# Optimization experiments

Measured on AMD Instinct MI355X. Metric: run time of the kernel, lower is better.

## Reference

```python
import jax, jax.numpy as jnp
import numpy as np

L, H, NH, B, S = 6, 768, 12, 4, 1024
D = H // NH
SCALE = 1.0 / np.sqrt(D)
EPS = 1e-5


def setup_inputs() -> dict:
    key = jax.random.key(0)
    ks = jax.random.split(key, 20)
    std = np.sqrt(2.0 / (5.0 * H)).astype(np.float32)
    w = lambda k, shape: (jax.random.normal(k, shape, jnp.float32) * std)
    x = jax.random.normal(ks[0], (B, S, H), jnp.float32)
    lengths = jnp.array([1024, 896, 768, 640])  # no fully-masked rows
    pad_mask = jnp.arange(S)[None, :] >= lengths[:, None]  # True = padding
    inp = {
        "x": x,
        "pad_mask": pad_mask,
        "Wq": w(ks[1], (L, H, H)), "bq": jnp.zeros((L, H), jnp.float32),
        "Wk": w(ks[2], (L, H, H)), "bk": w(ks[3], (L, H)) * 0.1,
        "Wv": w(ks[4], (L, H, H)), "bv": w(ks[5], (L, H)) * 0.1,
        "Wo": w(ks[6], (L, H, H)), "bo": jnp.zeros((L, H), jnp.float32),
        "ln1_g": jnp.ones((L, H), jnp.float32), "ln1_b": jnp.zeros((L, H), jnp.float32),
        "ln2_g": jnp.ones((L, H), jnp.float32), "ln2_b": jnp.zeros((L, H), jnp.float32),
        "W1": w(ks[7], (L, 8 * H, H)), "b1": jnp.zeros((L, 8 * H), jnp.float32),
        "W2": w(ks[8], (L, H, 4 * H)), "b2": jnp.zeros((L, H), jnp.float32),
        "out_g": jnp.ones((H,), jnp.float32), "out_b": jnp.zeros((H,), jnp.float32),
    }
    return inp


def _ln(x, g, b):
    m = jnp.mean(x, axis=-1, keepdims=True)
    v = jnp.mean(jnp.square(x - m), axis=-1, keepdims=True)
    return (x - m) * jax.lax.rsqrt(v + EPS) * g + b


def _encoder(x, pad_mask, params):
    def layer(x, p):
        (Wq, bq, Wk, bk, Wv, bv, Wo, bo, g1, be1, g2, be2, W1, b1, W2, b2) = p
        Bz, Sl, Hd = x.shape
        xn = _ln(x, g1, be1)
        q = (xn @ Wq.T + bq).reshape(Bz, Sl, NH, D)
        k = (xn @ Wk.T + bk).reshape(Bz, Sl, NH, D)
        v = (xn @ Wv.T + bv).reshape(Bz, Sl, NH, D)
        scores = jnp.einsum('bqhd,bkhd->bhqk', q, k) * SCALE
        scores = jnp.where(pad_mask[:, None, None, :], -jnp.inf, scores)
        probs = jax.nn.softmax(scores, axis=-1)
        av = jnp.einsum('bhqk,bkhd->bqhd', probs, v).reshape(Bz, Sl, Hd)
        x = x + (av @ Wo.T + bo)
        xn = _ln(x, g2, be2)
        h = xn @ W1.T + b1
        u, gate = jnp.split(h, 2, axis=-1)
        x = x + (u * jax.nn.gelu(gate, approximate=False)) @ W2.T + b2
        return x, None

    x, _ = jax.lax.scan(layer, x, params)
    return x


def reference(x, pad_mask, Wq, bq, Wk, bk, Wv, bv, Wo, bo,
              ln1_g, ln1_b, ln2_g, ln2_b, W1, b1, W2, b2, out_g, out_b):
    params = (Wq, bq, Wk, bk, Wv, bv, Wo, bo,
              ln1_g, ln1_b, ln2_g, ln2_b, W1, b1, W2, b2)
    x = _encoder(x, pad_mask, params)
    return _ln(x, out_g, out_b)
```

## Files before the change

### kernel.cpp

```cpp
#include <hip/hip_runtime.h>

typedef unsigned short u16;
typedef __bf16 bf16x8 __attribute__((ext_vector_type(8)));
typedef unsigned short us8 __attribute__((ext_vector_type(8)));
typedef unsigned short us4 __attribute__((ext_vector_type(4)));
typedef float f32x4 __attribute__((ext_vector_type(4)));

typedef __attribute__((address_space(3))) unsigned int as3_uint;
typedef const __attribute__((address_space(1))) unsigned int as1_cuint;

__device__ __forceinline__ u16 f2bf(float f) {
    unsigned u = __float_as_uint(f);
    u += 0x7FFFu + ((u >> 16) & 1u);
    return (u16)(u >> 16);
}
__device__ __forceinline__ float bf2f(u16 h) {
    return __uint_as_float(((unsigned)h) << 16);
}
__device__ __forceinline__ bf16x8 ld8(const u16* p) {
    return __builtin_bit_cast(bf16x8, *(const us8*)p);
}
#define MFMA16(a, b, c) __builtin_amdgcn_mfma_f32_16x16x32_bf16(a, b, c, 0, 0, 0)

__device__ __forceinline__ void glds16(const void* g, void* l) {
    __builtin_amdgcn_global_load_lds((as1_cuint*)g, (as3_uint*)l, 16, 0, 0);
}

__global__ void detect_k(const unsigned* __restrict__ pm, int* __restrict__ len4) {
    __shared__ int isbool;
    const int t = threadIdx.x;
    if (t == 0) isbool = 0;
    __syncthreads();
    unsigned orv = pm[t] | pm[256 + t] | pm[512 + t] | pm[768 + t];
    if (orv & 0xFFFFFF00u) atomicOr(&isbool, 1);
    __syncthreads();
    const int w = t >> 6, l = t & 63;
    int cnt = 0;
    if (isbool) {
        const unsigned char* p8 = (const unsigned char*)pm;
        for (int i = l; i < 1024; i += 64) cnt += (p8[w * 1024 + i] == 0) ? 1 : 0;
    } else {
        for (int i = l; i < 1024; i += 64) cnt += (pm[w * 1024 + i] == 0u) ? 1 : 0;
    }
#pragma unroll
    for (int m = 1; m < 64; m <<= 1) cnt += __shfl_xor(cnt, m);
    if (l == 0) {
        int c = cnt;
        if (c < 1) c = 1;
        if (c > 1024) c = 1024;
        len4[w] = c;
    }
}

__global__ __launch_bounds__(256) void conv_k(
    const float* __restrict__ Wq, const float* __restrict__ Wk,
    const float* __restrict__ Wv, const float* __restrict__ Wo,
    const float* __restrict__ W1, const float* __restrict__ W2,
    const float* __restrict__ bq, const float* __restrict__ bk,
    const float* __restrict__ bv,
    u16* __restrict__ wqkvo, u16* __restrict__ w1b, u16* __restrict__ w2b,
    float* __restrict__ bqkv, int lyr) {
    const int idx = blockIdx.x * 256 + threadIdx.x;
    const size_t e = (size_t)idx * 4;
    const float* src;
    u16* dst;
    if (e < 2359296u) {
        int which = (int)(e / 589824u);
        size_t off = e % 589824u;
        const float* m = (which == 0) ? Wq : (which == 1) ? Wk : (which == 2) ? Wv : Wo;
        src = m + (size_t)lyr * 589824u + off;
        dst = wqkvo + e;
    } else if (e < 7077888u) {
        size_t off = e - 2359296u;
        src = W1 + (size_t)lyr * 4718592u + off;
        dst = w1b + off;
    } else {
        size_t off = e - 7077888u;
        src = W2 + (size_t)lyr * 2359296u + off;
        dst = w2b + off;
    }
    float4 v = *(const float4*)src;
    us4 o;
    o[0] = f2bf(v.x); o[1] = f2bf(v.y); o[2] = f2bf(v.z); o[3] = f2bf(v.w);
    *(us4*)dst = o;
    if (idx < 2304) {
        float bb = (idx < 768) ? bq[lyr * 768 + idx]
                 : (idx < 1536) ? bk[lyr * 768 + idx - 768]
                                : bv[lyr * 768 + idx - 1536];
        bqkv[idx] = bb;
    }
}

template <int OUTF>
__global__ __launch_bounds__(256) void ln_k(const float* __restrict__ x,
                                            const float* __restrict__ gm,
                                            const float* __restrict__ bt,
                                            void* __restrict__ outp) {
    const int w = threadIdx.x >> 6, l = threadIdx.x & 63;
    const int row = blockIdx.x * 4 + w;
    const float4* xr = (const float4*)(x + (size_t)row * 768);
    float4 v[3];
    float s = 0.f, ss = 0.f;
#pragma unroll
    for (int i = 0; i < 3; ++i) {
        v[i] = xr[i * 64 + l];
        s += v[i].x + v[i].y + v[i].z + v[i].w;
        ss += v[i].x * v[i].x + v[i].y * v[i].y + v[i].z * v[i].z + v[i].w * v[i].w;
    }
#pragma unroll
    for (int m = 1; m < 64; m <<= 1) {
        s += __shfl_xor(s, m);
        ss += __shfl_xor(ss, m);
    }
    const float mean = s * (1.f / 768.f);
    float var = ss * (1.f / 768.f) - mean * mean;
    var = fmaxf(var, 0.f);
    const float rs = rsqrtf(var + 1e-5f);
    const float4* g4 = (const float4*)gm;
    const float4* b4 = (const float4*)bt;
#pragma unroll
    for (int i = 0; i < 3; ++i) {
        float4 gg = g4[i * 64 + l], bb = b4[i * 64 + l];
        float o0 = (v[i].x - mean) * rs * gg.x + bb.x;
        float o1 = (v[i].y - mean) * rs * gg.y + bb.y;
        float o2 = (v[i].z - mean) * rs * gg.z + bb.z;
        float o3 = (v[i].w - mean) * rs * gg.w + bb.w;
        if (OUTF) {
            ((float4*)outp)[(size_t)row * 192 + i * 64 + l] = make_float4(o0, o1, o2, o3);
        } else {
            us4 pk;
            pk[0] = f2bf(o0); pk[1] = f2bf(o1); pk[2] = f2bf(o2); pk[3] = f2bf(o3);
            ((us4*)outp)[(size_t)row * 192 + i * 64 + l] = pk;
        }
    }
}

template <int VAR, int NF, int CHAIN, int PRO>
__device__ __forceinline__ void g256_body(
    const u16* __restrict__ Ab, const u16* __restrict__ Bb0,
    const u16* __restrict__ Bb1,
    const u16* __restrict__ AbN, const u16* __restrict__ Bb0N,
    const u16* __restrict__ Bb1N,
    const float* __restrict__ bias, u16* __restrict__ outp,
    u16* __restrict__ vT, int ldout, int ncol0, int m0,
    u16 (&lds)[2][4][8192]) {
    const int tid = threadIdx.x;
    const int w = tid >> 6, l = tid & 63, ax = l & 15, gx = l >> 4;
    const int wr = w >> 2, wc = w & 3;
    const int K = 768;

    const int row0 = tid >> 2, cc0 = (tid & 3) ^ ((row0 >> 1) & 3);
    const int row1 = 128 + row0, cc1 = (tid & 3) ^ ((row1 >> 1) & 3);
    const size_t goA0 = (size_t)row0 * K + cc0 * 8;
    const size_t goA1 = (size_t)row1 * K + cc1 * 8;

    auto stage = [&](int u, int kt, int nxt) {
        const int kh = u & 1;
        const size_t koff = (size_t)kt * 64 + kh * 32;
        u16* d = (u16*)&lds[kt & 1][u][0];
        const u16* A_ = nxt ? AbN : Ab;
        const u16* B0_ = nxt ? Bb0N : Bb0;
        const u16* B1_ = nxt ? Bb1N : Bb1;
        if (u < 2) {
            glds16(A_ + goA0 + koff, d + tid * 8);
            glds16(A_ + goA1 + koff, d + (512 + tid) * 8);
        } else {
            glds16(B0_ + goA0 + koff, d + tid * 8);
            glds16(B1_ + goA1 + koff, d + (512 + tid) * 8);
        }
    };

    bf16x8 rav[4], rbv[NF];
    f32x4 acc[8][NF] = {};

    auto phase = [&](int buf, int q, int kh, int readB, int vm, int su, int skt,
                     int nxt) {
        if (vm == 8) asm volatile("s_waitcnt vmcnt(8)" ::: "memory");
        else if (vm == 4) asm volatile("s_waitcnt vmcnt(4)" ::: "memory");
        else if (vm == 0) asm volatile("s_waitcnt vmcnt(0)" ::: "memory");
        __builtin_amdgcn_s_barrier();
        if (readB) {
#pragma unroll
            for (int j = 0; j < NF; ++j) {
                int row;
                if (VAR == 0) row = wc * (16 * NF) + j * 16 + ax;
                else row = ((j >= NF / 2) ? 128 : 0) + wc * (8 * NF) +
                           (j % (NF / 2)) * 16 + ax;
                rbv[j] = ld8(&lds[buf][2 + kh][row * 32 + ((gx ^ ((row >> 1) & 3)) * 8)]);
            }
        }
#pragma unroll
        for (int mf = 0; mf < 4; ++mf) {
            int row = wr * 128 + q * 64 + mf * 16 + ax;
            rav[mf] = ld8(&lds[buf][kh][row * 32 + ((gx ^ ((row >> 1) & 3)) * 8)]);
        }
        if (su >= 0) stage(su, skt, nxt);
        asm volatile("s_waitcnt lgkmcnt(0)" ::: "memory");
        __builtin_amdgcn_sched_barrier(0);
        __builtin_amdgcn_s_setprio(1);
#pragma unroll
        for (int mf = 0; mf < 4; ++mf)
#pragma unroll
            for (int j = 0; j < NF; ++j)
                acc[q * 4 + mf][j] = MFMA16(rav[mf], rbv[j], acc[q * 4 + mf][j]);
        __builtin_amdgcn_s_setprio(0);
    };

    if (PRO) {
        stage(0, 0, 0); stage(2, 0, 0); stage(1, 0, 0);
        stage(3, 0, 0); stage(0, 1, 0); stage(2, 1, 0);
    }

#pragma unroll 1
    for (int t = 0; t < 5; ++t) {
        const int O = 2 * t + 1, E2 = 2 * t + 2, O2 = 2 * t + 3;
        phase(0, 0, 0, 1, 8, 1, O, 0);
        phase(0, 1, 0, 0, -1, 3, O, 0);
        phase(0, 0, 1, 1, 8, 0, E2, 0);
        phase(0, 1, 1, 0, -1, 2, E2, 0);
        phase(1, 0, 0, 1, 8, 1, E2, 0);
        phase(1, 1, 0, 0, -1, 3, E2, 0);
        phase(1, 0, 1, 1, 8, 0, O2, 0);
        phase(1, 1, 1, 0, -1, 2, O2, 0);
    }
    if (CHAIN) {
        phase(0, 0, 0, 1, 8, 1, 11, 0);
        phase(0, 1, 0, 0, -1, 3, 11, 0);
        phase(0, 0, 1, 1, 8, 0, 0, 1);
        phase(0, 1, 1, 0, -1, 2, 0, 1);
        phase(1, 0, 0, 1, 8, 1, 0, 1);
        phase(1, 1, 0, 0, -1, 3, 0, 1);
        phase(1, 0, 1, 1, 8, 0, 1, 1);
        phase(1, 1, 1, 0, -1, 2, 1, 1);
    } else {
        phase(0, 0, 0, 1, 8, 1, 11, 0);
        phase(0, 1, 0, 0, -1, 3, 11, 0);
        phase(0, 0, 1, 1, 8, -1, 0, 0);
        phase(0, 1, 1, 0, -1, -1, 0, 0);
        phase(1, 0, 0, 1, 4, -1, 0, 0);
        phase(1, 1, 0, 0, -1, -1, 0, 0);
        phase(1, 0, 1, 1, 0, -1, 0, 0);
        phase(1, 1, 1, 0, -1, -1, 0, 0);
    }

    const int rowb = m0 + wr * 128;
    if (VAR == 0) {
        if (ncol0 >= 1536) {
#pragma unroll
            for (int j = 0; j < NF; ++j) {
                const int col = ncol0 + wc * (16 * NF) + j * 16 + ax;
                const float bn = bias[col];
                u16* vcol = vT + (size_t)(col - 1536) * 4096;
#pragma unroll
                for (int am = 0; am < 8; ++am) {
                    const int rb_ = rowb + am * 16 + 4 * gx;
                    us4 pk;
#pragma unroll
                    for (int r = 0; r < 4; ++r) pk[r] = f2bf(acc[am][j][r] + bn);
                    *(us4*)(vcol + rb_) = pk;
                }
            }
        } else {
#pragma unroll
            for (int j = 0; j < NF; ++j) {
                const int col = ncol0 + wc * (16 * NF) + j * 16 + ax;
                const float bn = bias[col];
#pragma unroll
                for (int am = 0; am < 8; ++am) {
                    const int rb_ = rowb + am * 16 + 4 * gx;
#pragma unroll
                    for (int r = 0; r < 4; ++r)
                        outp[(size_t)(rb_ + r) * ldout + col] = f2bf(acc[am][j][r] + bn);
                }
            }
        }
    } else {
        const int P = NF / 2;
#pragma unroll
        for (int nf = 0; nf < NF / 2; ++nf) {
            const int col = ncol0 + wc * (16 * P) + nf * 16 + ax;
            const float bu_ = bias[col], bg_ = bias[3072 + col];
#pragma unroll
            for (int am = 0; am < 8; ++am) {
                const int rb_ = rowb + am * 16 + 4 * gx;
#pragma unroll
                for (int r = 0; r < 4; ++r) {
                    float uu = acc[am][nf][r] + bu_;
                    float gg = acc[am][P + nf][r] + bg_;
                    float gel = 0.5f * gg * (1.f + erff(gg * 0.70710678118f));
                    outp[(size_t)(rb_ + r) * ldout + col] = f2bf(uu * gel);
                }
            }
        }
    }
}

__global__ __launch_bounds__(512, 2) void qkv256_k(
    const u16* __restrict__ A, const u16* __restrict__ W,
    const float* __restrict__ bias, u16* __restrict__ outp,
    u16* __restrict__ vT) {
    __shared__ __align__(16) u16 lds[2][4][8192];
    const int bid = blockIdx.x;
    const int swz = (bid & 7) * 24 + (bid >> 3);
    const int nb = swz >> 4, mb = swz & 15;
    const int m0 = mb * 256;
    const u16* Ab = A + (size_t)m0 * 768;
    const u16* Bb0 = W + (size_t)(nb * 192) * 768;
    g256_body<0, 3, 0, 1>(Ab, Bb0, Bb0, nullptr, nullptr, nullptr,
                          bias, outp, vT, 2304, nb * 192, m0, lds);
}

__global__ __launch_bounds__(512, 2) void ffn1_k(
    const u16* __restrict__ A, const u16* __restrict__ W,
    const float* __restrict__ bias, u16* __restrict__ outp) {
    __shared__ __align__(16) u16 lds[2][4][8192];
    const int bid = blockIdx.x;
    const int swz = (bid & 7) * 32 + (bid >> 3);
    const int nb = swz >> 4, mb = swz & 15;
    const int m0 = mb * 256;
    const u16* Ab = A + (size_t)m0 * 768;
    const u16* Bb0 = W + (size_t)(nb * 128) * 768;
    const u16* Bb1 = W + (size_t)(3072 + nb * 128 - 128) * 768;
    const u16* Bb0h = W + (size_t)(2048 + nb * 64) * 768;
    const u16* Bb1h = W + (size_t)(5120 + nb * 64 - 128) * 768;
    g256_body<1, 4, 1, 1>(Ab, Bb0, Bb1, Ab, Bb0h, Bb1h,
                          bias, outp, nullptr, 3072, nb * 128, m0, lds);
    g256_body<1, 2, 0, 0>(Ab, Bb0h, Bb1h, nullptr, nullptr, nullptr,
                          bias, outp, nullptr, 3072, 2048 + nb * 64, m0, lds);
}

template <int EPI>
__global__ __launch_bounds__(512) void gemm_k(
    const u16* __restrict__ A, const u16* __restrict__ W,
    const float* __restrict__ bias, const float* __restrict__ resid,
    void* __restrict__ outp, int N, int K) {
    __shared__ __align__(16) u16 As[2][128 * 64];
    __shared__ __align__(16) u16 Bs[2][128 * 64];
    const int tid = threadIdx.x;
    const int w = tid >> 6, l = tid & 63, a = l & 15, g = l >> 4;
    const int wr = w >> 2, wc = w & 3;
    const int m0 = blockIdx.y * 128, n0 = blockIdx.x * 128;
    f32x4 acc[4][2] = {};
    const int nk = K >> 6;

    auto stage = [&](int kt, int buf) {
        const int k0 = kt * 64;
#pragma unroll
        for (int i = 0; i < 2; ++i) {
            int c = i * 512 + tid;
            int row = c >> 3, cc = c & 7, c8 = cc ^ (row & 7);
            glds16(A + (size_t)(m0 + row) * K + k0 + c8 * 8, &As[buf][c * 8]);
        }
#pragma unroll
        for (int i = 0; i < 2; ++i) {
            int c = i * 512 + tid;
            int row = c >> 3, cc = c & 7, c8 = cc ^ (row & 7);
            glds16(W + (size_t)(n0 + row) * K + k0 + c8 * 8, &Bs[buf][c * 8]);
        }
    };

    stage(0, 0);
    int cur = 0;
    for (int kt = 0; kt < nk; ++kt) {
        if (kt + 1 < nk) {
            stage(kt + 1, cur ^ 1);
            __builtin_amdgcn_sched_barrier(0);
            asm volatile("s_waitcnt vmcnt(4)" ::: "memory");
        } else {
            __builtin_amdgcn_sched_barrier(0);
            asm volatile("s_waitcnt vmcnt(0)" ::: "memory");
        }
        __builtin_amdgcn_s_barrier();
#pragma unroll
        for (int ks = 0; ks < 2; ++ks) {
            bf16x8 af[4], bv_[2];
#pragma unroll
            for (int m = 0; m < 4; ++m) {
                int row = wr * 64 + m * 16 + a;
                af[m] = ld8(&As[cur][row * 64 + (((ks * 4 + g) ^ (a & 7)) * 8)]);
            }
#pragma unroll
            for (int n = 0; n < 2; ++n) {
                int row = wc * 32 + n * 16 + a;
                bv_[n] = ld8(&Bs[cur][row * 64 + (((ks * 4 + g) ^ (a & 7)) * 8)]);
            }
#pragma unroll
            for (int m = 0; m < 4; ++m)
#pragma unroll
                for (int n = 0; n < 2; ++n)
                    acc[m][n] = MFMA16(af[m], bv_[n], acc[m][n]);
        }
        __builtin_amdgcn_s_barrier();
        cur ^= 1;
    }
    u16* outu = (u16*)outp;
    float* outf = (float*)outp;
    const int row0 = m0 + wr * 64, col0 = n0 + wc * 32;
#pragma unroll
    for (int n = 0; n < 2; ++n) {
        const int col = col0 + n * 16 + a;
        const float bn = bias[col];
#pragma unroll
        for (int m = 0; m < 4; ++m) {
            const int rb = row0 + m * 16 + 4 * g;
#pragma unroll
            for (int r = 0; r < 4; ++r) {
                const size_t off = (size_t)(rb + r) * N + col;
                float vv = acc[m][n][r] + bn;
                if constexpr (EPI == 0) {
                    outu[off] = f2bf(vv);
                } else {
                    outf[off] = vv + resid[off];
                }
            }
        }
    }
}

__global__ __launch_bounds__(256) void attn_k(const u16* __restrict__ qkv,
                                              const u16* __restrict__ vT,
                                              u16* __restrict__ av,
                                              const int* __restrict__ len4) {
    __shared__ __align__(16) u16 Ks[64 * 64];
    __shared__ __align__(16) u16 Vt[64 * 64];
    __shared__ __align__(16) u16 Ps[4][16 * 64];
    const int tid = threadIdx.x;
    const int w = tid >> 6, l = tid & 63, a = l & 15, g = l >> 4;
    const int qb = blockIdx.x, h = blockIdx.y, b = blockIdx.z;
    const size_t rowQ = (size_t)(b * 1024 + qb * 64 + w * 16 + a);
    const u16* qp = qkv + rowQ * 2304 + h * 64;
    bf16x8 qf[2];
    qf[0] = __builtin_bit_cast(bf16x8, *(const us8*)(qp + g * 8));
    qf[1] = __builtin_bit_cast(bf16x8, *(const us8*)(qp + 32 + g * 8));
    f32x4 O[4] = {};
    float m_r[4], l_r[4];
#pragma unroll
    for (int r = 0; r < 4; ++r) { m_r[r] = -1e30f; l_r[r] = 0.f; }
    const int length = len4[b];
    const int nkt = (length + 63) >> 6;
    for (int kt = 0; kt < nkt; ++kt) {
        __syncthreads();
#pragma unroll
        for (int i = 0; i < 2; ++i) {
            int c = i * 256 + tid;
            int row = c >> 3, cc = c & 7, c8 = cc ^ (row & 7);
            glds16(qkv + (size_t)(b * 1024 + kt * 64 + row) * 2304 + 768 + h * 64 + c8 * 8,
                   &Ks[c * 8]);
        }
        {
            const int d = l;
            const u16* vrow = vT + (size_t)(h * 64 + d) * 4096 + b * 1024 + kt * 64;
#pragma unroll
            for (int i = 0; i < 2; ++i) {
                int kkc = w + 4 * i;
                us8 vv = *(const us8*)(vrow + kkc * 8);
                int cc = kkc ^ (d & 7);
                *(us8*)&Vt[d * 64 + cc * 8] = vv;
            }
        }
        __syncthreads();
        f32x4 s[4] = {};
#pragma unroll
        for (int ks = 0; ks < 2; ++ks) {
#pragma unroll
            for (int f = 0; f < 4; ++f) {
                int row = f * 16 + a;
                bf16x8 kf = ld8(&Ks[row * 64 + (((ks * 4 + g) ^ (a & 7)) * 8)]);
                s[f] = MFMA16(qf[ks], kf, s[f]);
            }
        }
        float mloc[4] = {-1e30f, -1e30f, -1e30f, -1e30f};
#pragma unroll
        for (int f = 0; f < 4; ++f) {
            int kkg = kt * 64 + f * 16 + a;
            bool valid = kkg < length;
#pragma unroll
            for (int r = 0; r < 4; ++r) {
                float v = valid ? s[f][r] * 0.125f : -1e30f;
                s[f][r] = v;
                mloc[r] = fmaxf(mloc[r], v);
            }
        }
#pragma unroll
        for (int r = 0; r < 4; ++r) {
#pragma unroll
            for (int m = 1; m < 16; m <<= 1)
                mloc[r] = fmaxf(mloc[r], __shfl_xor(mloc[r], m));
        }
        float al[4], ps[4];
#pragma unroll
        for (int r = 0; r < 4; ++r) {
            float nm = fmaxf(m_r[r], mloc[r]);
            al[r] = __expf(m_r[r] - nm);
            m_r[r] = nm;
            ps[r] = 0.f;
        }
#pragma unroll
        for (int f = 0; f < 4; ++f)
#pragma unroll
            for (int r = 0; r < 4; ++r) {
                float p = __expf(s[f][r] - m_r[r]);
                s[f][r] = p;
                ps[r] += p;
            }
#pragma unroll
        for (int r = 0; r < 4; ++r) {
#pragma unroll
            for (int m = 1; m < 16; m <<= 1) ps[r] += __shfl_xor(ps[r], m);
            l_r[r] = l_r[r] * al[r] + ps[r];
        }
#pragma unroll
        for (int df = 0; df < 4; ++df)
#pragma unroll
            for (int r = 0; r < 4; ++r) O[df][r] *= al[r];
#pragma unroll
        for (int f = 0; f < 4; ++f)
#pragma unroll
            for (int r = 0; r < 4; ++r) {
                int prow = 4 * g + r;
                int cc = (2 * f + (a >> 3)) ^ (prow & 7);
                Ps[w][prow * 64 + cc * 8 + (a & 7)] = f2bf(s[f][r]);
            }
        asm volatile("s_waitcnt lgkmcnt(0)" ::: "memory");
        __builtin_amdgcn_sched_barrier(0);
#pragma unroll
        for (int ks = 0; ks < 2; ++ks) {
            bf16x8 pf = ld8(&Ps[w][a * 64 + (((ks * 4 + g) ^ (a & 7)) * 8)]);
#pragma unroll
            for (int df = 0; df < 4; ++df) {
                int vrow = df * 16 + a;
                bf16x8 vf = ld8(&Vt[vrow * 64 + (((ks * 4 + g) ^ (a & 7)) * 8)]);
                O[df] = MFMA16(pf, vf, O[df]);
            }
        }
    }
#pragma unroll
    for (int df = 0; df < 4; ++df) {
        int col = h * 64 + df * 16 + a;
#pragma unroll
        for (int r = 0; r < 4; ++r) {
            int row = b * 1024 + qb * 64 + w * 16 + 4 * g + r;
            av[(size_t)row * 768 + col] = f2bf(O[df][r] / l_r[r]);
        }
    }
}

extern "C" void kernel_launch(void* const* d_in, const int* in_sizes, int n_in,
                              void* d_out, int out_size, void* d_ws, size_t ws_size,
                              hipStream_t stream) {
    const float* x_in = (const float*)d_in[0];
    const unsigned* pm = (const unsigned*)d_in[1];
    const float* Wq = (const float*)d_in[2];
    const float* bq = (const float*)d_in[3];
    const float* Wk = (const float*)d_in[4];
    const float* bk = (const float*)d_in[5];
    const float* Wv = (const float*)d_in[6];
    const float* bv = (const float*)d_in[7];
    const float* Wo = (const float*)d_in[8];
    const float* bo = (const float*)d_in[9];
    const float* g1 = (const float*)d_in[10];
    const float* be1 = (const float*)d_in[11];
    const float* g2 = (const float*)d_in[12];
    const float* be2 = (const float*)d_in[13];
    const float* W1 = (const float*)d_in[14];
    const float* b1 = (const float*)d_in[15];
    const float* W2 = (const float*)d_in[16];
    const float* b2 = (const float*)d_in[17];
    const float* og = (const float*)d_in[18];
    const float* ob = (const float*)d_in[19];

    char* ws = (char*)d_ws;
    u16* wqkvo = (u16*)(ws + 0);
    u16* w1b   = (u16*)(ws + 4718592);
    u16* w2b   = (u16*)(ws + 14155776);
    float* bqkv = (float*)(ws + 18874368);
    int* len4  = (int*)(ws + 18883584);
    float* xbuf = (float*)(ws + 18883840);
    u16* xn    = (u16*)(ws + 31466752);
    u16* qkv   = (u16*)(ws + 37758208);
    u16* avb   = (u16*)(ws + 56632576);
    u16* ub    = (u16*)(ws + 62924032);
    u16* vT    = (u16*)(ws + 62924032);

    detect_k<<<1, 256, 0, stream>>>(pm, len4);
    for (int l = 0; l < 6; ++l) {
        conv_k<<<9216, 256, 0, stream>>>(Wq, Wk, Wv, Wo, W1, W2, bq, bk, bv,
                                         wqkvo, w1b, w2b, bqkv, l);
        const float* xcur = (l == 0) ? x_in : xbuf;
        ln_k<0><<<1024, 256, 0, stream>>>(xcur, g1 + l * 768, be1 + l * 768, xn);
        qkv256_k<<<192, 512, 0, stream>>>(xn, wqkvo, bqkv, qkv, vT);
        attn_k<<<dim3(16, 12, 4), 256, 0, stream>>>(qkv, vT, avb, len4);
        gemm_k<1><<<dim3(6, 32), 512, 0, stream>>>(avb, wqkvo + 3 * 589824, bo + l * 768,
                                                   xcur, xbuf, 768, 768);
        ln_k<0><<<1024, 256, 0, stream>>>(xbuf, g2 + l * 768, be2 + l * 768, xn);
        ffn1_k<<<256, 512, 0, stream>>>(xn, w1b, b1 + l * 6144, ub);
        gemm_k<1><<<dim3(6, 32), 512, 0, stream>>>(ub, w2b, b2 + l * 768, xbuf,
                                                   xbuf, 768, 3072);
    }
    ln_k<1><<<1024, 256, 0, stream>>>(xbuf, og, ob, d_out);
}
```

Measured before the change: 1.256 ms.

## Batch weight conversion, retile FFN1 as 1024-thread kernel, split-K gemm epilogue

All six layers' weights are now converted to bf16 in one launch before the layer loop, replacing six per-layer conversion launches, at the cost of a much larger workspace. FFN1 is rewritten as a single 1024-thread block that computes 256x192 up and gate tiles together, with a double-buffered LDS pipeline and a fused GELU epilogue. The output-projection and FFN2 gemm now split each 64-wide k-step across wave pairs, each wave holding a 64x64 tile, and the two partial sums are reduced through LDS before the epilogue. The aim is to cut launch overhead and raise MFMA density per LDS load, but it adds LDS round-trips and register pressure.

```diff
diff --git a/kernel.cpp b/kernel.cpp
--- a/kernel.cpp
+++ b/kernel.cpp
@@ -58,27 +58,22 @@
     const float* __restrict__ W1, const float* __restrict__ W2,
     const float* __restrict__ bq, const float* __restrict__ bk,
     const float* __restrict__ bv,
-    u16* __restrict__ wqkvo, u16* __restrict__ w1b, u16* __restrict__ w2b,
-    float* __restrict__ bqkv, int lyr) {
+    u16* __restrict__ wall, float* __restrict__ bqkv6) {
+    const int lyr = blockIdx.y;
     const int idx = blockIdx.x * 256 + threadIdx.x;
     const size_t e = (size_t)idx * 4;
     const float* src;
-    u16* dst;
     if (e < 2359296u) {
         int which = (int)(e / 589824u);
         size_t off = e % 589824u;
         const float* m = (which == 0) ? Wq : (which == 1) ? Wk : (which == 2) ? Wv : Wo;
         src = m + (size_t)lyr * 589824u + off;
-        dst = wqkvo + e;
     } else if (e < 7077888u) {
-        size_t off = e - 2359296u;
-        src = W1 + (size_t)lyr * 4718592u + off;
-        dst = w1b + off;
+        src = W1 + (size_t)lyr * 4718592u + (e - 2359296u);
     } else {
-        size_t off = e - 7077888u;
-        src = W2 + (size_t)lyr * 2359296u + off;
-        dst = w2b + off;
-    }
+        src = W2 + (size_t)lyr * 2359296u + (e - 7077888u);
+    }
+    u16* dst = wall + (size_t)lyr * 9437184u + e;
     float4 v = *(const float4*)src;
     us4 o;
     o[0] = f2bf(v.x); o[1] = f2bf(v.y); o[2] = f2bf(v.z); o[3] = f2bf(v.w);
@@ -87,7 +82,7 @@
         float bb = (idx < 768) ? bq[lyr * 768 + idx]
                  : (idx < 1536) ? bk[lyr * 768 + idx - 768]
                                 : bv[lyr * 768 + idx - 1536];
-        bqkv[idx] = bb;
+        bqkv6[lyr * 2304 + idx] = bb;
     }
 }
 
@@ -310,23 +305,95 @@
                           bias, outp, vT, 2304, nb * 192, m0, lds);
 }
 
-__global__ __launch_bounds__(512, 2) void ffn1_k(
+__global__ __launch_bounds__(1024, 1) void ffn1_k(
     const u16* __restrict__ A, const u16* __restrict__ W,
     const float* __restrict__ bias, u16* __restrict__ outp) {
-    __shared__ __align__(16) u16 lds[2][4][8192];
+    __shared__ __align__(16) u16 lds[2][40960];
+    const int tid = threadIdx.x;
+    const int w = tid >> 6, l = tid & 63, ax = l & 15, gx = l >> 4;
+    const int wr = w >> 2, wc = w & 3;
     const int bid = blockIdx.x;
     const int swz = (bid & 7) * 32 + (bid >> 3);
     const int nb = swz >> 4, mb = swz & 15;
     const int m0 = mb * 256;
     const u16* Ab = A + (size_t)m0 * 768;
-    const u16* Bb0 = W + (size_t)(nb * 128) * 768;
-    const u16* Bb1 = W + (size_t)(3072 + nb * 128 - 128) * 768;
-    const u16* Bb0h = W + (size_t)(2048 + nb * 64) * 768;
-    const u16* Bb1h = W + (size_t)(5120 + nb * 64 - 128) * 768;
-    g256_body<1, 4, 1, 1>(Ab, Bb0, Bb1, Ab, Bb0h, Bb1h,
-                          bias, outp, nullptr, 3072, nb * 128, m0, lds);
-    g256_body<1, 2, 0, 0>(Ab, Bb0h, Bb1h, nullptr, nullptr, nullptr,
-                          bias, outp, nullptr, 3072, 2048 + nb * 64, m0, lds);
+    const u16* Bu = W + (size_t)(nb * 192) * 768;
+    const u16* Bg = W + (size_t)(3072 + nb * 192) * 768;
+
+    const int ar0 = tid >> 3;
+    const int ac8 = ((tid & 7) ^ (ar0 & 7)) * 8;
+    const u16* As0 = Ab + (size_t)ar0 * 768 + ac8;
+    const u16* As1 = Ab + (size_t)(128 + ar0) * 768 + ac8;
+    const u16* Bs0 = Bu + (size_t)ar0 * 768 + ac8;
+    const u16* Bs1 = (ar0 < 64) ? Bu + (size_t)(128 + ar0) * 768 + ac8
+                                : Bg + (size_t)(ar0 - 64) * 768 + ac8;
+    const u16* Bs2 = Bg + (size_t)(64 + ar0) * 768 + ac8;
+
+    auto stage = [&](int kt) {
+        const size_t ko = (size_t)kt * 64;
+        u16* dA = &lds[kt & 1][0];
+        u16* dB = &lds[kt & 1][16384];
+        glds16(As0 + ko, dA + tid * 8);
+        glds16(As1 + ko, dA + (1024 + tid) * 8);
+        glds16(Bs0 + ko, dB + tid * 8);
+        glds16(Bs1 + ko, dB + (1024 + tid) * 8);
+        glds16(Bs2 + ko, dB + (2048 + tid) * 8);
+    };
+
+    f32x4 acc[4][6] = {};
+
+    auto phase = [&](int buf, int kh, int dost, int skt) {
+        if (kh == 0) asm volatile("s_waitcnt vmcnt(0)" ::: "memory");
+        __builtin_amdgcn_s_barrier();
+        bf16x8 rav[4], rbv[6];
+#pragma unroll
+        for (int j = 0; j < 6; ++j) {
+            int pr = ((j < 3) ? 0 : 192) + wc * 48 + (j % 3) * 16 + ax;
+            rbv[j] = ld8(&lds[buf][16384 + pr * 64 + (((kh * 4 + gx) ^ (pr & 7)) * 8)]);
+        }
+#pragma unroll
+        for (int mf = 0; mf < 4; ++mf) {
+            int row = wr * 64 + mf * 16 + ax;
+            rav[mf] = ld8(&lds[buf][row * 64 + (((kh * 4 + gx) ^ (row & 7)) * 8)]);
+        }
+        if (dost) stage(skt);
+        asm volatile("s_waitcnt lgkmcnt(0)" ::: "memory");
+        __builtin_amdgcn_sched_barrier(0);
+        __builtin_amdgcn_s_setprio(1);
+#pragma unroll
+        for (int mf = 0; mf < 4; ++mf)
+#pragma unroll
+            for (int j = 0; j < 6; ++j)
+                acc[mf][j] = MFMA16(rav[mf], rbv[j], acc[mf][j]);
+        __builtin_amdgcn_s_setprio(0);
+    };
+
+    stage(0);
+#pragma unroll 1
+    for (int kt = 0; kt < 11; ++kt) {
+        phase(kt & 1, 0, 1, kt + 1);
+        phase(kt & 1, 1, 0, 0);
+    }
+    phase(1, 0, 0, 0);
+    phase(1, 1, 0, 0);
+
+    const int rowb = m0 + wr * 64;
+#pragma unroll
+    for (int j = 0; j < 3; ++j) {
+        const int col = nb * 192 + wc * 48 + j * 16 + ax;
+        const float bu_ = bias[col], bg_ = bias[3072 + col];
+#pragma unroll
+        for (int mf = 0; mf < 4; ++mf) {
+            const int rb_ = rowb + mf * 16 + 4 * gx;
+#pragma unroll
+            for (int r = 0; r < 4; ++r) {
+                float uu = acc[mf][j][r] + bu_;
+                float gg = acc[mf][j + 3][r] + bg_;
+                float gel = 0.5f * gg * (1.f + erff(gg * 0.70710678118f));
+                outp[(size_t)(rb_ + r) * 3072 + col] = f2bf(uu * gel);
+            }
+        }
+    }
 }
 
 template <int EPI>
@@ -334,13 +401,12 @@
     const u16* __restrict__ A, const u16* __restrict__ W,
     const float* __restrict__ bias, const float* __restrict__ resid,
     void* __restrict__ outp, int N, int K) {
-    __shared__ __align__(16) u16 As[2][128 * 64];
-    __shared__ __align__(16) u16 Bs[2][128 * 64];
+    __shared__ __align__(16) u16 smem[4][128 * 64];
     const int tid = threadIdx.x;
     const int w = tid >> 6, l = tid & 63, a = l & 15, g = l >> 4;
-    const int wr = w >> 2, wc = w & 3;
+    const int wr = w >> 2, wc = (w >> 1) & 1, kz = w & 1;
     const int m0 = blockIdx.y * 128, n0 = blockIdx.x * 128;
-    f32x4 acc[4][2] = {};
+    f32x4 acc[4][4] = {};
     const int nk = K >> 6;
 
     auto stage = [&](int kt, int buf) {
@@ -349,13 +415,13 @@
         for (int i = 0; i < 2; ++i) {
             int c = i * 512 + tid;
             int row = c >> 3, cc = c & 7, c8 = cc ^ (row & 7);
-            glds16(A + (size_t)(m0 + row) * K + k0 + c8 * 8, &As[buf][c * 8]);
+            glds16(A + (size_t)(m0 + row) * K + k0 + c8 * 8, &smem[buf][c * 8]);
         }
 #pragma unroll
         for (int i = 0; i < 2; ++i) {
             int c = i * 512 + tid;
             int row = c >> 3, cc = c & 7, c8 = cc ^ (row & 7);
-            glds16(W + (size_t)(n0 + row) * K + k0 + c8 * 8, &Bs[buf][c * 8]);
+            glds16(W + (size_t)(n0 + row) * K + k0 + c8 * 8, &smem[2 + buf][c * 8]);
         }
     };
 
@@ -371,46 +437,65 @@
             asm volatile("s_waitcnt vmcnt(0)" ::: "memory");
         }
         __builtin_amdgcn_s_barrier();
-#pragma unroll
-        for (int ks = 0; ks < 2; ++ks) {
-            bf16x8 af[4], bv_[2];
-#pragma unroll
-            for (int m = 0; m < 4; ++m) {
-                int row = wr * 64 + m * 16 + a;
-                af[m] = ld8(&As[cur][row * 64 + (((ks * 4 + g) ^ (a & 7)) * 8)]);
-            }
-#pragma unroll
-            for (int n = 0; n < 2; ++n) {
-                int row = wc * 32 + n * 16 + a;
-                bv_[n] = ld8(&Bs[cur][row * 64 + (((ks * 4 + g) ^ (a & 7)) * 8)]);
-            }
-#pragma unroll
-            for (int m = 0; m < 4; ++m)
-#pragma unroll
-                for (int n = 0; n < 2; ++n)
-                    acc[m][n] = MFMA16(af[m], bv_[n], acc[m][n]);
-        }
+        bf16x8 af[4], bv_[4];
+#pragma unroll
+        for (int m = 0; m < 4; ++m) {
+            int row = wr * 64 + m * 16 + a;
+            af[m] = ld8(&smem[cur][row * 64 + (((kz * 4 + g) ^ (a & 7)) * 8)]);
+        }
+#pragma unroll
+        for (int n = 0; n < 4; ++n) {
+            int row = wc * 64 + n * 16 + a;
+            bv_[n] = ld8(&smem[2 + cur][row * 64 + (((kz * 4 + g) ^ (a & 7)) * 8)]);
+        }
+        asm volatile("s_waitcnt lgkmcnt(0)" ::: "memory");
+        __builtin_amdgcn_sched_barrier(0);
+        __builtin_amdgcn_s_setprio(1);
+#pragma unroll
+        for (int m = 0; m < 4; ++m)
+#pragma unroll
+            for (int n = 0; n < 4; ++n)
+                acc[m][n] = MFMA16(af[m], bv_[n], acc[m][n]);
+        __builtin_amdgcn_s_setprio(0);
         __builtin_amdgcn_s_barrier();
         cur ^= 1;
     }
-    u16* outu = (u16*)outp;
-    float* outf = (float*)outp;
-    const int row0 = m0 + wr * 64, col0 = n0 + wc * 32;
-#pragma unroll
-    for (int n = 0; n < 2; ++n) {
-        const int col = col0 + n * 16 + a;
-        const float bn = bias[col];
-#pragma unroll
-        for (int m = 0; m < 4; ++m) {
-            const int rb = row0 + m * 16 + 4 * g;
-#pragma unroll
-            for (int r = 0; r < 4; ++r) {
-                const size_t off = (size_t)(rb + r) * N + col;
-                float vv = acc[m][n][r] + bn;
-                if constexpr (EPI == 0) {
-                    outu[off] = f2bf(vv);
-                } else {
-                    outf[off] = vv + resid[off];
+
+    __syncthreads();
+    float* sc = (float*)&smem[0][0];
+    const int quad = wr * 2 + wc;
+    if (kz == 1) {
+#pragma unroll
+        for (int m = 0; m < 4; ++m)
+#pragma unroll
+            for (int n = 0; n < 4; ++n)
+#pragma unroll
+                for (int r = 0; r < 4; ++r)
+                    sc[quad * 4096 + (m * 16 + 4 * g + r) * 64 + n * 16 + a] =
+                        acc[m][n][r];
+    }
+    __syncthreads();
+    if (kz == 0) {
+        u16* outu = (u16*)outp;
+        float* outf = (float*)outp;
+        const int row0 = m0 + wr * 64, col0 = n0 + wc * 64;
+#pragma unroll
+        for (int n = 0; n < 4; ++n) {
+            const int col = col0 + n * 16 + a;
+            const float bn = bias[col];
+#pragma unroll
+            for (int m = 0; m < 4; ++m) {
+                const int rb = row0 + m * 16 + 4 * g;
+#pragma unroll
+                for (int r = 0; r < 4; ++r) {
+                    const size_t off = (size_t)(rb + r) * N + col;
+                    float vv = acc[m][n][r] + bn +
+                               sc[quad * 4096 + (m * 16 + 4 * g + r) * 64 + n * 16 + a];
+                    if constexpr (EPI == 0) {
+                        outu[off] = f2bf(vv);
+                    } else {
+                        outf[off] = vv + resid[off];
+                    }
                 }
             }
         }
@@ -570,31 +655,30 @@
     const float* ob = (const float*)d_in[19];
 
     char* ws = (char*)d_ws;
-    u16* wqkvo = (u16*)(ws + 0);
-    u16* w1b   = (u16*)(ws + 4718592);
-    u16* w2b   = (u16*)(ws + 14155776);
-    float* bqkv = (float*)(ws + 18874368);
-    int* len4  = (int*)(ws + 18883584);
-    float* xbuf = (float*)(ws + 18883840);
-    u16* xn    = (u16*)(ws + 31466752);
-    u16* qkv   = (u16*)(ws + 37758208);
-    u16* avb   = (u16*)(ws + 56632576);
-    u16* ub    = (u16*)(ws + 62924032);
-    u16* vT    = (u16*)(ws + 62924032);
+    u16* wall  = (u16*)(ws + 0);
+    float* bqkv6 = (float*)(ws + 113246208);
+    int* len4  = (int*)(ws + 113301504);
+    float* xbuf = (float*)(ws + 113301760);
+    u16* xn    = (u16*)(ws + 125884672);
+    u16* qkv   = (u16*)(ws + 132176128);
+    u16* avb   = (u16*)(ws + 151050496);
+    u16* ub    = (u16*)(ws + 157341952);
+    u16* vT    = (u16*)(ws + 157341952);
 
     detect_k<<<1, 256, 0, stream>>>(pm, len4);
+    conv_k<<<dim3(9216, 6), 256, 0, stream>>>(Wq, Wk, Wv, Wo, W1, W2, bq, bk, bv,
+                                              wall, bqkv6);
     for (int l = 0; l < 6; ++l) {
-        conv_k<<<9216, 256, 0, stream>>>(Wq, Wk, Wv, Wo, W1, W2, bq, bk, bv,
-                                         wqkvo, w1b, w2b, bqkv, l);
+        u16* wl = wall + (size_t)l * 9437184u;
         const float* xcur = (l == 0) ? x_in : xbuf;
         ln_k<0><<<1024, 256, 0, stream>>>(xcur, g1 + l * 768, be1 + l * 768, xn);
-        qkv256_k<<<192, 512, 0, stream>>>(xn, wqkvo, bqkv, qkv, vT);
+        qkv256_k<<<192, 512, 0, stream>>>(xn, wl, bqkv6 + l * 2304, qkv, vT);
         attn_k<<<dim3(16, 12, 4), 256, 0, stream>>>(qkv, vT, avb, len4);
-        gemm_k<1><<<dim3(6, 32), 512, 0, stream>>>(avb, wqkvo + 3 * 589824, bo + l * 768,
+        gemm_k<1><<<dim3(6, 32), 512, 0, stream>>>(avb, wl + 3 * 589824, bo + l * 768,
                                                    xcur, xbuf, 768, 768);
         ln_k<0><<<1024, 256, 0, stream>>>(xbuf, g2 + l * 768, be2 + l * 768, xn);
-        ffn1_k<<<256, 512, 0, stream>>>(xn, w1b, b1 + l * 6144, ub);
-        gemm_k<1><<<dim3(6, 32), 512, 0, stream>>>(ub, w2b, b2 + l * 768, xbuf,
+        ffn1_k<<<256, 1024, 0, stream>>>(xn, wl + 2359296, b1 + l * 6144, ub);
+        gemm_k<1><<<dim3(6, 32), 512, 0, stream>>>(ub, wl + 7077888, b2 + l * 768, xbuf,
                                                    xbuf, 768, 3072);
     }
     ln_k<1><<<1024, 256, 0, stream>>>(xbuf, og, ob, d_out);
```

Measured after the change: 1.847 ms. 47.1% more time.
